# Kernel tuning notes

Hardware: AMD Instinct MI355X
Metric: run time of the kernel (lower is better)

Reference implementation:

```python
import jax, jax.numpy as jnp
import numpy as np


def setup_inputs() -> dict:
    key = jax.random.key(0)
    k1, k2, k3, k4 = jax.random.split(key, 4)
    B, N, d_in, d_out = 8, 2048, 256, 256
    x = jax.random.normal(k1, (B, N, d_in), dtype=jnp.float32)
    adj_hat = jax.random.uniform(k2, (B, N, N), dtype=jnp.float32)
    W = jax.random.normal(k3, (d_out, d_in), dtype=jnp.float32) * (1.0 / np.sqrt(d_in))
    b = jax.random.normal(k4, (d_out,), dtype=jnp.float32) * 0.01
    return {"x": x, "adj_hat": adj_hat, "W": W, "b": b}


def reference(x, adj_hat, W, b):
    # Degrees from adj = adj_hat - I (i.e. without self loops): row sum minus diagonal.
    N = adj_hat.shape[1]
    diag = jnp.diagonal(adj_hat, axis1=-2, axis2=-1)          # [B, N]
    d = adj_hat.sum(axis=-1) - diag                           # [B, N]
    d_inv_sqrt = jnp.power(d, -0.5)                           # [B, N]
    # dad = D^-1/2 @ adj_hat @ D^-1/2  ==  d_i * a_ij * d_j (elementwise broadcast)
    dad = d_inv_sqrt[:, :, None] * adj_hat * d_inv_sqrt[:, None, :]  # [B, N, N]
    h = jnp.einsum('bnd,od->bno', x, W) + b                   # projection [B, N, d_out]
    return jnp.einsum('bnm,bmo->bno', dad, h)                 # [B, N, d_out]
```

## Files before the change

### kernel.cpp

```cpp
#include <hip/hip_runtime.h>
#include <hip/hip_bf16.h>


#define BATCH 8
#define NN    2048
#define DIN   256
#define DOUT  256
#define RTOT  (BATCH * NN)
#define AP    (NN + 32)
#define HP    (RTOT + 32)

typedef short  bf16x8  __attribute__((ext_vector_type(8)));
typedef short  short4v __attribute__((ext_vector_type(4)));
typedef float  f32x4   __attribute__((ext_vector_type(4)));

__device__ __forceinline__ short f2bf(float f) {
    union { float f; unsigned u; } v; v.f = f;
    unsigned r = v.u + 0x7fffu + ((v.u >> 16) & 1u);
    return (short)(r >> 16);
}

__device__ __forceinline__ void gl_lds16(const unsigned short* g, unsigned short* l) {
    __builtin_amdgcn_global_load_lds(
        (const __attribute__((address_space(1))) unsigned int*)g,
        (__attribute__((address_space(3))) unsigned int*)l, 16, 0, 0);
}

__global__ __launch_bounds__(256) void k_degree_cvt(const float* __restrict__ adj,
                                                    float* __restrict__ dis,
                                                    unsigned short* __restrict__ abf) {
    const int row = blockIdx.x;
    const int n = row & (NN - 1);
    const int tid = threadIdx.x;
    const float4* rp4 = (const float4*)(adj + (size_t)row * NN);
    unsigned short* op = abf + (size_t)row * AP;

    float s = 0.f;
#pragma unroll
    for (int i = 0; i < 2; i++) {
        float4 v = rp4[tid + i * 256];
        s += (v.x + v.y) + (v.z + v.w);
        short4v sv = { f2bf(v.x), f2bf(v.y), f2bf(v.z), f2bf(v.w) };
        *(short4v*)(op + 4 * (tid + i * 256)) = sv;
    }
#pragma unroll
    for (int off = 32; off; off >>= 1) s += __shfl_down(s, off);
    __shared__ float red[4];
    if ((tid & 63) == 0) red[tid >> 6] = s;
    __syncthreads();
    if (tid == 0) {
        float tot  = (red[0] + red[1]) + (red[2] + red[3]);
        float diag = ((const float*)rp4)[n];
        dis[row]   = rsqrtf(tot - diag);
    }
}

__global__ __launch_bounds__(256) void k_proj(const float* __restrict__ x,
                                              const float* __restrict__ W,
                                              const float* __restrict__ bias,
                                              const float* __restrict__ dis,
                                              unsigned short* __restrict__ hT) {
    const int mt  = blockIdx.y;
    const int nt  = blockIdx.x;
    const int tid = threadIdx.x;
    const int w = tid >> 6, lane = tid & 63;
    const int wr = w >> 1, wc = w & 1;
    const int l16 = lane & 15, quad = lane >> 4;

    __shared__ short As[128][32];
    __shared__ short Bs[128][32];

    f32x4 acc[4][4];
#pragma unroll
    for (int i = 0; i < 4; i++)
#pragma unroll
        for (int j = 0; j < 4; j++) acc[i][j] = (f32x4){0.f, 0.f, 0.f, 0.f};

    const float4* Wf4 = (const float4*)(W + (size_t)mt * 128 * DIN);
    const float4* Xf4 = (const float4*)(x + (size_t)nt * 128 * DIN);

    for (int kk = 0; kk < DIN / 32; kk++) {
        const int k0 = kk * 32;
        __syncthreads();
#pragma unroll
        for (int it = 0; it < 4; it++) {
            int idx = tid + it * 256;
            int r = idx >> 3, c = idx & 7;
            float4 va = Wf4[(size_t)r * (DIN / 4) + (k0 >> 2) + c];
            float4 vb = Xf4[(size_t)r * (DIN / 4) + (k0 >> 2) + c];
            short4v sa = { f2bf(va.x), f2bf(va.y), f2bf(va.z), f2bf(va.w) };
            short4v sb = { f2bf(vb.x), f2bf(vb.y), f2bf(vb.z), f2bf(vb.w) };
            *(short4v*)&As[r][c * 4] = sa;
            *(short4v*)&Bs[r][c * 4] = sb;
        }
        __syncthreads();
        bf16x8 af[4], bfv[4];
#pragma unroll
        for (int i = 0; i < 4; i++) af[i]  = *(bf16x8*)&As[wr * 64 + i * 16 + l16][quad * 8];
#pragma unroll
        for (int j = 0; j < 4; j++) bfv[j] = *(bf16x8*)&Bs[wc * 64 + j * 16 + l16][quad * 8];
#pragma unroll
        for (int i = 0; i < 4; i++)
#pragma unroll
            for (int j = 0; j < 4; j++)
                acc[i][j] = __builtin_amdgcn_mfma_f32_16x16x32_bf16(af[i], bfv[j], acc[i][j], 0, 0, 0);
    }

#pragma unroll
    for (int i = 0; i < 4; i++) {
        const int orow_base = mt * 128 + wr * 64 + i * 16 + quad * 4;
#pragma unroll
        for (int r = 0; r < 4; r++) {
            const int orow = orow_base + r;
            const float bb = bias[orow];
#pragma unroll
            for (int j = 0; j < 4; j++) {
                const int col = nt * 128 + wc * 64 + j * 16 + l16;
                float v = (acc[i][j][r] + bb) * dis[col];
                hT[(size_t)orow * HP + col] = (unsigned short)f2bf(v);
            }
        }
    }
}

__global__ __launch_bounds__(256, 2) void k_main(const unsigned short* __restrict__ abf,
                                                 const unsigned short* __restrict__ hT,
                                                 const float* __restrict__ dis,
                                                 float* __restrict__ out) {
    const int bx    = blockIdx.x;
    const int b     = bx & 7;
    const int mtile = (bx >> 3) & 31;
    const int ctile = bx >> 8;
    const int n0    = mtile * 64;
    const int tid  = threadIdx.x;
    const int w    = tid >> 6, lane = tid & 63;
    const int l16  = lane & 15, quad = lane >> 4;
    const int lr   = lane >> 2;
    const int lc   = (lane & 3) * 8;

    __shared__ short As[4][64][32];
    __shared__ short Bs[4][128][32];

    const unsigned short* agp  = abf + (size_t)(b * NN + n0 + w * 16 + lr) * AP + lc;
    const unsigned short* bgp0 = hT + (size_t)(ctile * 128 + w * 32 + lr) * HP + b * NN + lc;
    const unsigned short* bgp1 = bgp0 + (size_t)16 * HP;

    f32x4 acc[4][2];
#pragma unroll
    for (int i = 0; i < 4; i++)
#pragma unroll
        for (int j = 0; j < 2; j++) acc[i][j] = (f32x4){0.f, 0.f, 0.f, 0.f};

    for (int g = 0; g < NN / 128; g++) {
#pragma unroll
        for (int s = 0; s < 4; s++) {
            const int ko = g * 128 + s * 32;
            gl_lds16(agp + ko,  (unsigned short*)&As[s][w * 16][0]);
            gl_lds16(bgp0 + ko, (unsigned short*)&Bs[s][w * 32][0]);
            gl_lds16(bgp1 + ko, (unsigned short*)&Bs[s][w * 32 + 16][0]);
        }
        __syncthreads();
#pragma unroll
        for (int s = 0; s < 4; s++) {
            bf16x8 af[4], bfv[2];
#pragma unroll
            for (int i = 0; i < 4; i++) af[i]  = *(bf16x8*)&As[s][i * 16 + l16][quad * 8];
#pragma unroll
            for (int j = 0; j < 2; j++) bfv[j] = *(bf16x8*)&Bs[s][w * 32 + j * 16 + l16][quad * 8];
#pragma unroll
            for (int i = 0; i < 4; i++)
#pragma unroll
                for (int j = 0; j < 2; j++)
                    acc[i][j] = __builtin_amdgcn_mfma_f32_16x16x32_bf16(af[i], bfv[j], acc[i][j], 0, 0, 0);
        }
        __syncthreads();
    }

    const float* disb = dis + (size_t)b * NN;
#pragma unroll
    for (int i = 0; i < 4; i++) {
#pragma unroll
        for (int r = 0; r < 4; r++) {
            const int nrow = n0 + i * 16 + quad * 4 + r;
            const float dn = disb[nrow];
#pragma unroll
            for (int j = 0; j < 2; j++) {
                const int ocol = ctile * 128 + w * 32 + j * 16 + l16;
                out[((size_t)b * NN + nrow) * DOUT + ocol] = dn * acc[i][j][r];
            }
        }
    }
}

extern "C" void kernel_launch(void* const* d_in, const int* in_sizes, int n_in,
                              void* d_out, int out_size, void* d_ws, size_t ws_size,
                              hipStream_t stream) {
    const float* x    = (const float*)d_in[0];
    const float* adj  = (const float*)d_in[1];
    const float* W    = (const float*)d_in[2];
    const float* bias = (const float*)d_in[3];
    float* out = (float*)d_out;

    float* dis = (float*)d_ws;
    unsigned short* hT  = (unsigned short*)((char*)d_ws + 65536);
    unsigned short* abf = (unsigned short*)((char*)d_ws + 65536 + (size_t)DOUT * HP * 2);

    k_degree_cvt<<<RTOT, 256, 0, stream>>>(adj, dis, abf);
    k_proj<<<dim3(128, 2), 256, 0, stream>>>(x, W, bias, dis, hT);
    k_main<<<512, 256, 0, stream>>>(abf, hT, dis, out);
}
```

Baseline: 259.9 us.

## Double-buffer LDS tiles in main GEMM and register-prefetch in projection

The main aggregation kernel now splits its LDS into two 64-wide k buffers. It issues the direct global-to-LDS loads for the next step before computing on the current one, so memory latency overlaps the MFMA work instead of sitting behind a load-then-barrier pattern. The projection kernel prefetches the next fp32 slice of W and x into registers while the current slice is in use. This costs extra registers in k_proj and more loop iterations and barriers in k_main. Total LDS use is unchanged.

```diff
diff --git a/kernel.cpp b/kernel.cpp
--- a/kernel.cpp
+++ b/kernel.cpp
@@ -79,21 +79,40 @@
     const float4* Wf4 = (const float4*)(W + (size_t)mt * 128 * DIN);
     const float4* Xf4 = (const float4*)(x + (size_t)nt * 128 * DIN);
 
+    const int idx_r = tid >> 3;
+    const int idx_c = tid & 7;
+
+    float4 va[4], vb[4];
+#pragma unroll
+    for (int it = 0; it < 4; it++) {
+        int idx = tid + it * 256;
+        int r = idx >> 3, c = idx & 7;
+        va[it] = Wf4[(size_t)r * (DIN / 4) + c];
+        vb[it] = Xf4[(size_t)r * (DIN / 4) + c];
+    }
+    (void)idx_r; (void)idx_c;
+
     for (int kk = 0; kk < DIN / 32; kk++) {
-        const int k0 = kk * 32;
         __syncthreads();
 #pragma unroll
         for (int it = 0; it < 4; it++) {
             int idx = tid + it * 256;
             int r = idx >> 3, c = idx & 7;
-            float4 va = Wf4[(size_t)r * (DIN / 4) + (k0 >> 2) + c];
-            float4 vb = Xf4[(size_t)r * (DIN / 4) + (k0 >> 2) + c];
-            short4v sa = { f2bf(va.x), f2bf(va.y), f2bf(va.z), f2bf(va.w) };
-            short4v sb = { f2bf(vb.x), f2bf(vb.y), f2bf(vb.z), f2bf(vb.w) };
+            short4v sa = { f2bf(va[it].x), f2bf(va[it].y), f2bf(va[it].z), f2bf(va[it].w) };
+            short4v sb = { f2bf(vb[it].x), f2bf(vb[it].y), f2bf(vb[it].z), f2bf(vb[it].w) };
             *(short4v*)&As[r][c * 4] = sa;
             *(short4v*)&Bs[r][c * 4] = sb;
         }
         __syncthreads();
+        if (kk < DIN / 32 - 1) {
+#pragma unroll
+            for (int it = 0; it < 4; it++) {
+                int idx = tid + it * 256;
+                int r = idx >> 3, c = idx & 7;
+                va[it] = Wf4[(size_t)r * (DIN / 4) + (kk + 1) * 8 + c];
+                vb[it] = Xf4[(size_t)r * (DIN / 4) + (kk + 1) * 8 + c];
+            }
+        }
         bf16x8 af[4], bfv[4];
 #pragma unroll
         for (int i = 0; i < 4; i++) af[i]  = *(bf16x8*)&As[wr * 64 + i * 16 + l16][quad * 8];
@@ -138,8 +157,8 @@
     const int lr   = lane >> 2;
     const int lc   = (lane & 3) * 8;
 
-    __shared__ short As[4][64][32];
-    __shared__ short Bs[4][128][32];
+    __shared__ short As[2][2][64][32];
+    __shared__ short Bs[2][2][128][32];
 
     const unsigned short* agp  = abf + (size_t)(b * NN + n0 + w * 16 + lr) * AP + lc;
     const unsigned short* bgp0 = hT + (size_t)(ctile * 128 + w * 32 + lr) * HP + b * NN + lc;
@@ -151,22 +170,32 @@
 #pragma unroll
         for (int j = 0; j < 2; j++) acc[i][j] = (f32x4){0.f, 0.f, 0.f, 0.f};
 
-    for (int g = 0; g < NN / 128; g++) {
-#pragma unroll
-        for (int s = 0; s < 4; s++) {
-            const int ko = g * 128 + s * 32;
-            gl_lds16(agp + ko,  (unsigned short*)&As[s][w * 16][0]);
-            gl_lds16(bgp0 + ko, (unsigned short*)&Bs[s][w * 32][0]);
-            gl_lds16(bgp1 + ko, (unsigned short*)&Bs[s][w * 32 + 16][0]);
-        }
-        __syncthreads();
-#pragma unroll
-        for (int s = 0; s < 4; s++) {
+#pragma unroll
+    for (int s = 0; s < 2; s++) {
+        gl_lds16(agp + s * 32,  (unsigned short*)&As[0][s][w * 16][0]);
+        gl_lds16(bgp0 + s * 32, (unsigned short*)&Bs[0][s][w * 32][0]);
+        gl_lds16(bgp1 + s * 32, (unsigned short*)&Bs[0][s][w * 32 + 16][0]);
+    }
+    __syncthreads();
+
+    for (int t = 0; t < NN / 64; t++) {
+        const int cur = t & 1;
+        if (t < NN / 64 - 1) {
+            const int ko = (t + 1) * 64;
+#pragma unroll
+            for (int s = 0; s < 2; s++) {
+                gl_lds16(agp + ko + s * 32,  (unsigned short*)&As[cur ^ 1][s][w * 16][0]);
+                gl_lds16(bgp0 + ko + s * 32, (unsigned short*)&Bs[cur ^ 1][s][w * 32][0]);
+                gl_lds16(bgp1 + ko + s * 32, (unsigned short*)&Bs[cur ^ 1][s][w * 32 + 16][0]);
+            }
+        }
+#pragma unroll
+        for (int s = 0; s < 2; s++) {
             bf16x8 af[4], bfv[2];
 #pragma unroll
-            for (int i = 0; i < 4; i++) af[i]  = *(bf16x8*)&As[s][i * 16 + l16][quad * 8];
-#pragma unroll
-            for (int j = 0; j < 2; j++) bfv[j] = *(bf16x8*)&Bs[s][w * 32 + j * 16 + l16][quad * 8];
+            for (int i = 0; i < 4; i++) af[i]  = *(bf16x8*)&As[cur][s][i * 16 + l16][quad * 8];
+#pragma unroll
+            for (int j = 0; j < 2; j++) bfv[j] = *(bf16x8*)&Bs[cur][s][w * 32 + j * 16 + l16][quad * 8];
 #pragma unroll
             for (int i = 0; i < 4; i++)
 #pragma unroll
```

Result: slower. 268.6 us (+3.4%).

## Double-buffer LDS tiles in main aggregation kernel to overlap loads with MFMA

Applied to the files above, without the earlier changes.

Replaces the load-all-then-compute loop over 128-wide K chunks with a two-stage pipeline over 64-wide chunks. Asynchronous global-to-LDS loads for the next stage are issued before the current buffer is consumed, and explicit vmcnt/lgkmcnt waits plus raw barriers replace __syncthreads. Total LDS use is unchanged. The aim is to hide global memory latency behind MFMA work. The cost is more barriers per K and tighter reliance on hand-counted wait counters.

```diff
diff --git a/kernel.cpp b/kernel.cpp
--- a/kernel.cpp
+++ b/kernel.cpp
@@ -138,8 +138,8 @@
     const int lr   = lane >> 2;
     const int lc   = (lane & 3) * 8;
 
-    __shared__ short As[4][64][32];
-    __shared__ short Bs[4][128][32];
+    __shared__ short As[2][2][64][32];
+    __shared__ short Bs[2][2][128][32];
 
     const unsigned short* agp  = abf + (size_t)(b * NN + n0 + w * 16 + lr) * AP + lc;
     const unsigned short* bgp0 = hT + (size_t)(ctile * 128 + w * 32 + lr) * HP + b * NN + lc;
@@ -151,30 +151,52 @@
 #pragma unroll
         for (int j = 0; j < 2; j++) acc[i][j] = (f32x4){0.f, 0.f, 0.f, 0.f};
 
-    for (int g = 0; g < NN / 128; g++) {
-#pragma unroll
-        for (int s = 0; s < 4; s++) {
-            const int ko = g * 128 + s * 32;
-            gl_lds16(agp + ko,  (unsigned short*)&As[s][w * 16][0]);
-            gl_lds16(bgp0 + ko, (unsigned short*)&Bs[s][w * 32][0]);
-            gl_lds16(bgp1 + ko, (unsigned short*)&Bs[s][w * 32 + 16][0]);
-        }
-        __syncthreads();
-#pragma unroll
-        for (int s = 0; s < 4; s++) {
-            bf16x8 af[4], bfv[2];
-#pragma unroll
-            for (int i = 0; i < 4; i++) af[i]  = *(bf16x8*)&As[s][i * 16 + l16][quad * 8];
-#pragma unroll
-            for (int j = 0; j < 2; j++) bfv[j] = *(bf16x8*)&Bs[s][w * 32 + j * 16 + l16][quad * 8];
-#pragma unroll
-            for (int i = 0; i < 4; i++)
-#pragma unroll
-                for (int j = 0; j < 2; j++)
-                    acc[i][j] = __builtin_amdgcn_mfma_f32_16x16x32_bf16(af[i], bfv[j], acc[i][j], 0, 0, 0);
-        }
-        __syncthreads();
-    }
+#define STAGE(T, BUF)                                                              \
+    do {                                                                           \
+        const int ko_ = (T) * 64;                                                  \
+        _Pragma("unroll")                                                          \
+        for (int s_ = 0; s_ < 2; s_++) {                                           \
+            gl_lds16(agp  + ko_ + s_ * 32, (unsigned short*)&As[BUF][s_][w * 16][0]);      \
+            gl_lds16(bgp0 + ko_ + s_ * 32, (unsigned short*)&Bs[BUF][s_][w * 32][0]);      \
+            gl_lds16(bgp1 + ko_ + s_ * 32, (unsigned short*)&Bs[BUF][s_][w * 32 + 16][0]); \
+        }                                                                          \
+    } while (0)
+
+#define COMPUTE(BUF)                                                               \
+    do {                                                                           \
+        _Pragma("unroll")                                                          \
+        for (int s = 0; s < 2; s++) {                                              \
+            bf16x8 af[4], bfv[2];                                                  \
+            _Pragma("unroll")                                                      \
+            for (int i = 0; i < 4; i++) af[i]  = *(bf16x8*)&As[BUF][s][i * 16 + l16][quad * 8];        \
+            _Pragma("unroll")                                                      \
+            for (int j = 0; j < 2; j++) bfv[j] = *(bf16x8*)&Bs[BUF][s][w * 32 + j * 16 + l16][quad * 8]; \
+            _Pragma("unroll")                                                      \
+            for (int i = 0; i < 4; i++)                                            \
+                _Pragma("unroll")                                                  \
+                for (int j = 0; j < 2; j++)                                        \
+                    acc[i][j] = __builtin_amdgcn_mfma_f32_16x16x32_bf16(af[i], bfv[j], acc[i][j], 0, 0, 0); \
+        }                                                                          \
+    } while (0)
+
+    STAGE(0, 0);
+    STAGE(1, 1);
+
+    for (int t = 0; t < NN / 64 - 1; t++) {
+        const int cur = t & 1;
+        asm volatile("s_waitcnt vmcnt(6)" ::: "memory");
+        __builtin_amdgcn_s_barrier();
+        COMPUTE(cur);
+        asm volatile("s_waitcnt lgkmcnt(0)" ::: "memory");
+        __builtin_amdgcn_s_barrier();
+        if (t + 2 < NN / 64) STAGE(t + 2, cur);
+    }
+    asm volatile("s_waitcnt vmcnt(0)" ::: "memory");
+    __builtin_amdgcn_s_barrier();
+    COMPUTE(1);
+
+#undef STAGE
+#undef COMPUTE
 
     const float* disb = dis + (size_t)b * NN;
 #pragma unroll
```

After: 260.1 us. Within noise of the previous version (+0.1%).

## Fuse adjacency bf16 conversion into main GEMM loads, dropping the intermediate buffer

Applied to the files above, without the earlier changes.

The degree kernel no longer writes a padded bf16 copy of the adjacency matrix. The main GEMM now reads fp32 adjacency rows directly into registers, converts them to bf16 and stores them to shared memory, while the hT tile keeps using direct global-to-LDS loads. This removes a large intermediate write and its re-read. In exchange, each of the two output-column tiles re-reads fp32 adjacency, which is twice as many bytes per read unless the cache absorbs it. The A-operand loads are also now synchronous register loads with conversion work inside the loop.

```diff
diff --git a/kernel.cpp b/kernel.cpp
--- a/kernel.cpp
+++ b/kernel.cpp
@@ -7,7 +7,6 @@
 #define DIN   256
 #define DOUT  256
 #define RTOT  (BATCH * NN)
-#define AP    (NN + 32)
 #define HP    (RTOT + 32)
 
 typedef short  bf16x8  __attribute__((ext_vector_type(8)));
@@ -26,22 +25,18 @@
         (__attribute__((address_space(3))) unsigned int*)l, 16, 0, 0);
 }
 
-__global__ __launch_bounds__(256) void k_degree_cvt(const float* __restrict__ adj,
-                                                    float* __restrict__ dis,
-                                                    unsigned short* __restrict__ abf) {
+__global__ __launch_bounds__(256) void k_degree(const float* __restrict__ adj,
+                                                float* __restrict__ dis) {
     const int row = blockIdx.x;
     const int n = row & (NN - 1);
     const int tid = threadIdx.x;
     const float4* rp4 = (const float4*)(adj + (size_t)row * NN);
-    unsigned short* op = abf + (size_t)row * AP;
 
     float s = 0.f;
 #pragma unroll
     for (int i = 0; i < 2; i++) {
         float4 v = rp4[tid + i * 256];
         s += (v.x + v.y) + (v.z + v.w);
-        short4v sv = { f2bf(v.x), f2bf(v.y), f2bf(v.z), f2bf(v.w) };
-        *(short4v*)(op + 4 * (tid + i * 256)) = sv;
     }
 #pragma unroll
     for (int off = 32; off; off >>= 1) s += __shfl_down(s, off);
@@ -123,7 +118,7 @@
     }
 }
 
-__global__ __launch_bounds__(256, 2) void k_main(const unsigned short* __restrict__ abf,
+__global__ __launch_bounds__(256, 2) void k_main(const float* __restrict__ adj,
                                                  const unsigned short* __restrict__ hT,
                                                  const float* __restrict__ dis,
                                                  float* __restrict__ out) {
@@ -141,7 +136,7 @@
     __shared__ short As[4][64][32];
     __shared__ short Bs[4][128][32];
 
-    const unsigned short* agp  = abf + (size_t)(b * NN + n0 + w * 16 + lr) * AP + lc;
+    const float4* agf4 = (const float4*)(adj + (size_t)(b * NN + n0 + w * 16 + lr) * NN + lc);
     const unsigned short* bgp0 = hT + (size_t)(ctile * 128 + w * 32 + lr) * HP + b * NN + lc;
     const unsigned short* bgp1 = bgp0 + (size_t)16 * HP;
 
@@ -155,9 +150,20 @@
 #pragma unroll
         for (int s = 0; s < 4; s++) {
             const int ko = g * 128 + s * 32;
-            gl_lds16(agp + ko,  (unsigned short*)&As[s][w * 16][0]);
             gl_lds16(bgp0 + ko, (unsigned short*)&Bs[s][w * 32][0]);
             gl_lds16(bgp1 + ko, (unsigned short*)&Bs[s][w * 32 + 16][0]);
+        }
+        float4 av0[4], av1[4];
+#pragma unroll
+        for (int s = 0; s < 4; s++) {
+            av0[s] = agf4[g * 32 + s * 8];
+            av1[s] = agf4[g * 32 + s * 8 + 1];
+        }
+#pragma unroll
+        for (int s = 0; s < 4; s++) {
+            bf16x8 pk = { f2bf(av0[s].x), f2bf(av0[s].y), f2bf(av0[s].z), f2bf(av0[s].w),
+                          f2bf(av1[s].x), f2bf(av1[s].y), f2bf(av1[s].z), f2bf(av1[s].w) };
+            *(bf16x8*)&As[s][w * 16 + lr][lc] = pk;
         }
         __syncthreads();
 #pragma unroll
@@ -203,9 +209,8 @@
 
     float* dis = (float*)d_ws;
     unsigned short* hT  = (unsigned short*)((char*)d_ws + 65536);
-    unsigned short* abf = (unsigned short*)((char*)d_ws + 65536 + (size_t)DOUT * HP * 2);
-
-    k_degree_cvt<<<RTOT, 256, 0, stream>>>(adj, dis, abf);
+
+    k_degree<<<RTOT, 256, 0, stream>>>(adj, dis);
     k_proj<<<dim3(128, 2), 256, 0, stream>>>(x, W, bias, dis, hT);
-    k_main<<<512, 256, 0, stream>>>(abf, hT, dis, out);
-}
+    k_main<<<512, 256, 0, stream>>>(adj, hT, dis, out);
+}
```

After: 254.0 us. 1.02x faster.
